# Kernel optimization log

Hardware: AMD Instinct MI355X
Metric: run time of the kernel (lower is better)

## Reference

```python
import jax, jax.numpy as jnp
import numpy as np

N = 100000   # nodes
E = 3200000  # edges
HIGH, LOW, EMB, HID, OUT = 384, 64, 128, 128, 2

def setup_inputs() -> dict:
    key = jax.random.key(0)
    ks = jax.random.split(key, 12)
    def lin(k, fan_in, fan_out):
        bound = 1.0 / np.sqrt(fan_in)
        kw, kb = jax.random.split(k)
        W = jax.random.uniform(kw, (fan_in, fan_out), jnp.float32, -bound, bound)
        b = jax.random.uniform(kb, (fan_out,), jnp.float32, -bound, bound)
        return W, b
    W_emb, b_emb = lin(ks[0], LOW, EMB)
    W1, b1 = lin(ks[1], HIGH + EMB, HID)
    W2, b2 = lin(ks[2], HID, HID)
    W_lin, b_lin = lin(ks[3], HID, OUT)
    return {
        "high_dim_features": jax.random.normal(ks[4], (N, HIGH), jnp.float32),
        "low_dim_features": jax.random.normal(ks[5], (N, LOW), jnp.float32),
        "edge_index": jax.random.randint(ks[6], (2, E), 0, N, jnp.int32),
        "W_emb": W_emb, "b_emb": b_emb,
        "W1": W1, "b1": b1,
        "W2": W2, "b2": b2,
        "W_lin": W_lin, "b_lin": b_lin,
    }

def _gcn_conv(x, W, b, src, dst, dis):
    # GCNConv: add self-loops, symmetric normalization D^-1/2 (A+I) D^-1/2
    xl = x @ W                                   # [N, out]
    norm = dis[src] * dis[dst]                   # [E]
    agg = jax.ops.segment_sum(xl[src] * norm[:, None], dst, num_segments=N)
    agg = agg + xl * (dis * dis)[:, None]        # self-loop term
    return agg + b

def reference(high_dim_features, low_dim_features, edge_index,
              W_emb, b_emb, W1, b1, W2, b2, W_lin, b_lin):
    src, dst = edge_index[0], edge_index[1]
    # degree with self-loops, computed on destination nodes (PyG default)
    deg = jax.ops.segment_sum(jnp.ones((E,), jnp.float32), dst, num_segments=N) + 1.0
    dis = jax.lax.rsqrt(deg)                     # deg >= 1 always

    low_emb = jax.nn.relu(low_dim_features @ W_emb + b_emb)
    x = jnp.concatenate([high_dim_features, low_emb], axis=1)  # [N, HIGH+EMB]
    x = jax.nn.relu(_gcn_conv(x, W1, b1, src, dst, dis))
    # dropout is identity in eval mode
    x = jax.nn.relu(_gcn_conv(x, W2, b2, src, dst, dis))
    x = x @ W_lin + b_lin
    return jax.nn.log_softmax(x, axis=1)
```

## Files before the change

### kernel.cpp

```cpp
#include <hip/hip_runtime.h>

#define HIGH 384
#define LOWD 64
#define EMB  128
#define HID  128

#define BINSHIFT 8
#define SRCBITS  17
#define SRCMASK  0x1FFFF
#define NBLK     256

typedef unsigned int u32;
typedef unsigned short u16;
typedef unsigned char u8;
typedef __attribute__((ext_vector_type(8))) short bf16x8;
typedef __attribute__((ext_vector_type(4))) float f32x4;
typedef __attribute__((ext_vector_type(2))) float f32x2;

__device__ __forceinline__ u32 pack_bf16(float a, float b) {
    u32 ua = __builtin_bit_cast(u32, a);
    u32 ub = __builtin_bit_cast(u32, b);
    ua += 0x7fffu + ((ua >> 16) & 1u);
    ub += 0x7fffu + ((ub >> 16) & 1u);
    return (ua >> 16) | (ub & 0xffff0000u);
}
__device__ __forceinline__ u16 pack1_bf16(float a) {
    u32 ua = __builtin_bit_cast(u32, a);
    ua += 0x7fffu + ((ua >> 16) & 1u);
    return (u16)(ua >> 16);
}
__device__ __forceinline__ u8 pack1_fp8(float a) {
    int r = __builtin_amdgcn_cvt_pk_fp8_f32(a, a, 0, false);
    return (u8)(r & 0xff);
}


__global__ void k_dis(const int* __restrict__ cnt, float* __restrict__ dis, int N) {
    int i = blockIdx.x * 256 + threadIdx.x;
    if (i < N) dis[i] = rsqrtf((float)cnt[i] + 1.0f);
}

__global__ void k_castw_all(const float* __restrict__ W1, u16* __restrict__ Wt1,
                            const float* __restrict__ W2, u16* __restrict__ Wt2,
                            const float* __restrict__ WE, u16* __restrict__ WtE) {
    int i = blockIdx.x * 256 + threadIdx.x;
    if (i < 65536) {
        int k = i >> 7, c = i & 127;
        Wt1[c * 512 + k] = pack1_bf16(W1[i]);
    } else if (i < 81920) {
        int j = i - 65536;
        int k = j >> 7, c = j & 127;
        Wt2[c * 128 + k] = pack1_bf16(W2[j]);
    } else if (i < 90112) {
        int j = i - 81920;
        int k = j >> 7, c = j & 127;
        WtE[c * 64 + k] = pack1_bf16(WE[j]);
    }
}


__global__ __launch_bounds__(256) void k_binhist(const int* __restrict__ dst, int E,
                                                 int* __restrict__ cnts, int NB) {
    __shared__ int hist[512];
    for (int b = threadIdx.x; b < NB; b += 256) hist[b] = 0;
    __syncthreads();
    int CH = (E + gridDim.x - 1) / gridDim.x;
    int e0 = blockIdx.x * CH;
    int e1 = min(E, e0 + CH);
    for (int e = e0 + threadIdx.x; e < e1; e += 256)
        atomicAdd(&hist[dst[e] >> BINSHIFT], 1);
    __syncthreads();
    for (int b = threadIdx.x; b < NB; b += 256)
        cnts[b * NBLK + blockIdx.x] = hist[b];
}

__global__ __launch_bounds__(256) void k_binscatter(const int* __restrict__ src,
                                                    const int* __restrict__ dst, int E,
                                                    const int* __restrict__ cnts,
                                                    u32* __restrict__ packed, int NB) {
    __shared__ int cur[512];
    for (int b = threadIdx.x; b < NB; b += 256) cur[b] = cnts[b * NBLK + blockIdx.x];
    __syncthreads();
    int CH = (E + gridDim.x - 1) / gridDim.x;
    int e0 = blockIdx.x * CH;
    int e1 = min(E, e0 + CH);
    for (int e = e0 + threadIdx.x; e < e1; e += 256) {
        int d = dst[e];
        int s = src[e];
        int bin = d >> BINSHIFT;
        int pos = atomicAdd(&cur[bin], 1);
        packed[pos] = (u32)s | ((u32)(d & 255) << SRCBITS);
    }
}

__global__ __launch_bounds__(256) void k_hist2(const u32* __restrict__ packed,
                                               const int* __restrict__ cnts, int E,
                                               int* __restrict__ cnt, int NB, int N) {
    __shared__ int hist[256];
    int t = threadIdx.x;
    hist[t] = 0;
    __syncthreads();
    int b = blockIdx.x;
    int begin = cnts[b * NBLK];
    int end = (b + 1 < NB) ? cnts[(b + 1) * NBLK] : E;
    for (int e = begin + t; e < end; e += 256)
        atomicAdd(&hist[packed[e] >> SRCBITS], 1);
    __syncthreads();
    int idx = (b << BINSHIFT) + t;
    if (idx < N) cnt[idx] = hist[t];
}

__global__ __launch_bounds__(256) void k_fill2(const u32* __restrict__ packed,
                                               const int* __restrict__ cnts, int E,
                                               const int* __restrict__ row_start,
                                               int* __restrict__ csr, int NB, int N) {
    __shared__ int cur[256];
    int t = threadIdx.x;
    int b = blockIdx.x;
    int base = b << BINSHIFT;
    cur[t] = row_start[min(base + t, N)];
    __syncthreads();
    int begin = cnts[b * NBLK];
    int end = (b + 1 < NB) ? cnts[(b + 1) * NBLK] : E;
    for (int e = begin + t; e < end; e += 256) {
        u32 p = packed[e];
        int pos = atomicAdd(&cur[p >> SRCBITS], 1);
        csr[pos] = (int)((p & SRCMASK) << 5);
    }
}


__global__ void k_scan1(const int* __restrict__ in, int n, int* __restrict__ bsums) {
    __shared__ int sh[256];
    int t = threadIdx.x;
    int base = blockIdx.x * 1024 + t * 4;
    int s = 0;
#pragma unroll
    for (int j = 0; j < 4; j++) { int idx = base + j; s += (idx < n) ? in[idx] : 0; }
    sh[t] = s; __syncthreads();
    for (int off = 128; off > 0; off >>= 1) {
        if (t < off) sh[t] += sh[t + off];
        __syncthreads();
    }
    if (t == 0) bsums[blockIdx.x] = sh[0];
}

__global__ void k_scan2(int* bsums, int nb) {
    if (threadIdx.x == 0 && blockIdx.x == 0) {
        int run = 0;
        for (int i = 0; i < nb; i++) { int v = bsums[i]; bsums[i] = run; run += v; }
    }
}

__global__ void k_scan3_flat(int* __restrict__ data, int n, const int* __restrict__ bsums) {
    __shared__ int sh[256];
    int t = threadIdx.x;
    int base = blockIdx.x * 1024 + t * 4;
    int v[4]; int s = 0;
#pragma unroll
    for (int j = 0; j < 4; j++) { int idx = base + j; v[j] = (idx < n) ? data[idx] : 0; s += v[j]; }
    sh[t] = s; __syncthreads();
    int x = s;
    for (int off = 1; off < 256; off <<= 1) {
        int y = (t >= off) ? sh[t - off] : 0;
        __syncthreads();
        x += y; sh[t] = x;
        __syncthreads();
    }
    int run = bsums[blockIdx.x] + (x - s);
#pragma unroll
    for (int j = 0; j < 4; j++) {
        int idx = base + j;
        if (idx < n) data[idx] = run;
        run += v[j];
    }
}

__global__ void k_scan3_rows(const int* __restrict__ cnt, int N, const int* __restrict__ bsums,
                             int* __restrict__ row_start, int E) {
    __shared__ int sh[256];
    int t = threadIdx.x;
    int base = blockIdx.x * 1024 + t * 4;
    int v[4]; int s = 0;
#pragma unroll
    for (int j = 0; j < 4; j++) { int idx = base + j; v[j] = (idx < N) ? cnt[idx] : 0; s += v[j]; }
    sh[t] = s; __syncthreads();
    int x = s;
    for (int off = 1; off < 256; off <<= 1) {
        int y = (t >= off) ? sh[t - off] : 0;
        __syncthreads();
        x += y; sh[t] = x;
        __syncthreads();
    }
    int run = bsums[blockIdx.x] + (x - s);
#pragma unroll
    for (int j = 0; j < 4; j++) {
        int idx = base + j;
        if (idx < N) row_start[idx] = run;
        run += v[j];
    }
    if (blockIdx.x == 0 && t == 0) row_start[N] = E;
}


template<bool A1BF, bool BIAS, bool RELU, bool SCALE, int OUT>
__global__ __launch_bounds__(256, 6) void k_mgemm(
    const void* __restrict__ A1v, int K1,
    const u32* __restrict__ A2, int K2,
    const u16* __restrict__ Wt,
    const float* __restrict__ bias,
    const float* __restrict__ dis,
    void* __restrict__ Cv, int M)
{
    __shared__ u32 Als[2][64][16];
    __shared__ u32 Bls[2][128][16];

    const int tid = threadIdx.x;
    const int l = tid & 63;
    const int w = tid >> 6;
    const int g = l >> 4;
    const int lr = l & 15;
    const int blockRow = blockIdx.x * 64;
    const int K = K1 + K2;
    const int T = K >> 5;

    const int ar = tid >> 2;
    const int ak = tid & 3;
    int arow = blockRow + ar; if (arow >= M) arow = M - 1;
    const int awb = (ak + ((ar >> 1) & 3)) & 3;

    const int wc = tid >> 1;
    const int wh = tid & 1;
    const int wsw = (wc >> 1) & 3;
    const int wb0 = (wh * 2 + wsw) & 3;
    const int wb1 = (wh * 2 + 1 + wsw) & 3;

    const float* a1f = (const float*)A1v + (size_t)arow * K1;
    const u32*   a1b = (const u32*)A1v + (size_t)arow * (K1 >> 1);
    const u32*   a2b = A2 + (size_t)arow * (K2 >> 1);
    const u32*   wtb = (const u32*)Wt + (size_t)wc * (K >> 1);

    f32x4 acc[8];
#pragma unroll
    for (int j = 0; j < 8; j++) acc[j] = (f32x4)0.f;

    u32 pa[4], wk[8];

    auto load_tile = [&](int k0) {
        if (k0 < K1) {
            if (A1BF) {
                uint4 a = *(const uint4*)(a1b + (k0 >> 1) + ak * 4);
                pa[0] = a.x; pa[1] = a.y; pa[2] = a.z; pa[3] = a.w;
            } else {
                const float* src = a1f + k0 + ak * 8;
                float4 f0 = *(const float4*)(src + 0);
                float4 f1 = *(const float4*)(src + 4);
                pa[0] = pack_bf16(f0.x, f0.y); pa[1] = pack_bf16(f0.z, f0.w);
                pa[2] = pack_bf16(f1.x, f1.y); pa[3] = pack_bf16(f1.z, f1.w);
            }
        } else {
            uint4 a = *(const uint4*)(a2b + ((k0 - K1) >> 1) + ak * 4);
            pa[0] = a.x; pa[1] = a.y; pa[2] = a.z; pa[3] = a.w;
        }
        const u32* srcw = wtb + ((k0 + wh * 16) >> 1);
        uint4 a = *(const uint4*)srcw;
        uint4 b = *(const uint4*)(srcw + 4);
        wk[0] = a.x; wk[1] = a.y; wk[2] = a.z; wk[3] = a.w;
        wk[4] = b.x; wk[5] = b.y; wk[6] = b.z; wk[7] = b.w;
    };
    auto store_tile = [&](int buf) {
        *(uint4*)&Als[buf][ar][awb * 4] = make_uint4(pa[0], pa[1], pa[2], pa[3]);
        *(uint4*)&Bls[buf][wc][wb0 * 4] = make_uint4(wk[0], wk[1], wk[2], wk[3]);
        *(uint4*)&Bls[buf][wc][wb1 * 4] = make_uint4(wk[4], wk[5], wk[6], wk[7]);
    };

    load_tile(0);
    store_tile(0);
    __syncthreads();

    for (int t = 0; t < T; t++) {
        const int cur = t & 1;
        const bool more = (t + 1 < T);
        if (more) load_tile((t + 1) << 5);

        bf16x8 af;
        {
            int r = w * 16 + lr;
            int blk = (g + ((r >> 1) & 3)) & 3;
            af = *(const bf16x8*)&Als[cur][r][blk * 4];
        }
#pragma unroll
        for (int cb = 0; cb < 8; cb++) {
            int c = cb * 16 + lr;
            int blk = (g + ((c >> 1) & 3)) & 3;
            bf16x8 bf = *(const bf16x8*)&Bls[cur][c][blk * 4];
            acc[cb] = __builtin_amdgcn_mfma_f32_16x16x32_bf16(af, bf, acc[cb], 0, 0, 0);
        }
        if (more) store_tile(cur ^ 1);
        __syncthreads();
    }

    float disv[4];
    if (SCALE) {
#pragma unroll
        for (int j = 0; j < 4; j++) {
            int row = blockRow + w * 16 + g * 4 + j;
            disv[j] = (row < M) ? dis[row] : 0.f;
        }
    }
#pragma unroll
    for (int cb = 0; cb < 8; cb++) {
        int col = cb * 16 + lr;
        float bv = BIAS ? bias[col] : 0.f;
#pragma unroll
        for (int j = 0; j < 4; j++) {
            int row = blockRow + w * 16 + g * 4 + j;
            if (row < M) {
                float v = acc[cb][j];
                if (BIAS) v += bv;
                if (SCALE) v *= disv[j];
                if (RELU) v = fmaxf(v, 0.f);
                if (OUT == 0) {
                    ((u16*)Cv)[(size_t)row * 128 + col] = pack1_bf16(v);
                } else {
                    ((u8*)Cv)[(size_t)row * 128 + col] = pack1_fp8(v);
                }
            }
        }
    }
}


template<int MODE>
__global__ __launch_bounds__(256) void k_gatherw(
    const u32* __restrict__ xls32, const int* __restrict__ row_start,
    const int* __restrict__ csr, const float* __restrict__ dis,
    const float* __restrict__ bias, const float* __restrict__ Wl,
    const float* __restrict__ bl, void* __restrict__ outv, int N)
{
    int wave = threadIdx.x >> 6;
    int lane = threadIdx.x & 63;
    int half = lane >> 5;
    int w32 = lane & 31;
    int n = blockIdx.x * 4 + wave;
    if (n >= N) return;
    int jb = row_start[n], je = row_start[n + 1];

    float a0 = 0.f, a1 = 0.f, a2 = 0.f, a3 = 0.f;
    {
        u32 v = xls32[(u32)n * 32 + w32];
        if (half == 0) {
            f32x2 lo = __builtin_amdgcn_cvt_pk_f32_fp8((int)v, false);
            f32x2 hi = __builtin_amdgcn_cvt_pk_f32_fp8((int)v, true);
            a0 = lo.x; a1 = lo.y; a2 = hi.x; a3 = hi.y;
        }
    }

    int j = jb;
    for (; j + 7 < je; j += 8) {
        int c0 = csr[j + 4 * half + 0];
        int c1 = csr[j + 4 * half + 1];
        int c2 = csr[j + 4 * half + 2];
        int c3 = csr[j + 4 * half + 3];
        u32 v0 = xls32[(u32)c0 + w32];
        u32 v1 = xls32[(u32)c1 + w32];
        u32 v2 = xls32[(u32)c2 + w32];
        u32 v3 = xls32[(u32)c3 + w32];
        f32x2 l0 = __builtin_amdgcn_cvt_pk_f32_fp8((int)v0, false);
        f32x2 h0 = __builtin_amdgcn_cvt_pk_f32_fp8((int)v0, true);
        f32x2 l1 = __builtin_amdgcn_cvt_pk_f32_fp8((int)v1, false);
        f32x2 h1 = __builtin_amdgcn_cvt_pk_f32_fp8((int)v1, true);
        f32x2 l2 = __builtin_amdgcn_cvt_pk_f32_fp8((int)v2, false);
        f32x2 h2 = __builtin_amdgcn_cvt_pk_f32_fp8((int)v2, true);
        f32x2 l3 = __builtin_amdgcn_cvt_pk_f32_fp8((int)v3, false);
        f32x2 h3 = __builtin_amdgcn_cvt_pk_f32_fp8((int)v3, true);
        a0 += (l0.x + l1.x) + (l2.x + l3.x);
        a1 += (l0.y + l1.y) + (l2.y + l3.y);
        a2 += (h0.x + h1.x) + (h2.x + h3.x);
        a3 += (h0.y + h1.y) + (h2.y + h3.y);
    }
    for (; j + 3 < je; j += 4) {
        int c0 = csr[j + 2 * half];
        int c1 = csr[j + 2 * half + 1];
        u32 v0 = xls32[(u32)c0 + w32];
        u32 v1 = xls32[(u32)c1 + w32];
        f32x2 l0 = __builtin_amdgcn_cvt_pk_f32_fp8((int)v0, false);
        f32x2 h0 = __builtin_amdgcn_cvt_pk_f32_fp8((int)v0, true);
        f32x2 l1 = __builtin_amdgcn_cvt_pk_f32_fp8((int)v1, false);
        f32x2 h1 = __builtin_amdgcn_cvt_pk_f32_fp8((int)v1, true);
        a0 += l0.x + l1.x; a1 += l0.y + l1.y;
        a2 += h0.x + h1.x; a3 += h0.y + h1.y;
    }
    if (j + 1 < je) {
        int c = csr[j + half];
        u32 v = xls32[(u32)c + w32];
        f32x2 lo = __builtin_amdgcn_cvt_pk_f32_fp8((int)v, false);
        f32x2 hi = __builtin_amdgcn_cvt_pk_f32_fp8((int)v, true);
        a0 += lo.x; a1 += lo.y; a2 += hi.x; a3 += hi.y;
        j += 2;
    }
    if (j < je) {
        int c = csr[j];
        u32 v = xls32[(u32)c + w32];
        if (half == 0) {
            f32x2 lo = __builtin_amdgcn_cvt_pk_f32_fp8((int)v, false);
            f32x2 hi = __builtin_amdgcn_cvt_pk_f32_fp8((int)v, true);
            a0 += lo.x; a1 += lo.y; a2 += hi.x; a3 += hi.y;
        }
    }

    a0 += __shfl(a0, w32 + 32);
    a1 += __shfl(a1, w32 + 32);
    a2 += __shfl(a2, w32 + 32);
    a3 += __shfl(a3, w32 + 32);

    float d = dis[n];
    float4 bv = *(const float4*)&bias[w32 * 4];
    float h0v = fmaxf(fmaf(d, a0, bv.x), 0.f);
    float h1v = fmaxf(fmaf(d, a1, bv.y), 0.f);
    float h2v = fmaxf(fmaf(d, a2, bv.z), 0.f);
    float h3v = fmaxf(fmaf(d, a3, bv.w), 0.f);

    if (MODE == 0) {
        if (half == 0) {
            uint2 pw;
            pw.x = pack_bf16(h0v, h1v);
            pw.y = pack_bf16(h2v, h3v);
            *(uint2*)((u32*)outv + (size_t)n * 64 + w32 * 2) = pw;
        }
    } else {
        float4 q0 = *(const float4*)&Wl[w32 * 8];
        float4 q1 = *(const float4*)&Wl[w32 * 8 + 4];
        float p0 = h0v * q0.x + h1v * q0.z + h2v * q1.x + h3v * q1.z;
        float p1 = h0v * q0.y + h1v * q0.w + h2v * q1.y + h3v * q1.w;
#pragma unroll
        for (int off = 16; off > 0; off >>= 1) {
            p0 += __shfl_down(p0, off);
            p1 += __shfl_down(p1, off);
        }
        if (lane == 0) {
            float z0 = p0 + bl[0], z1 = p1 + bl[1];
            float m = fmaxf(z0, z1);
            float ls = m + logf(expf(z0 - m) + expf(z1 - m));
            float* out = (float*)outv;
            out[(size_t)n * 2 + 0] = z0 - ls;
            out[(size_t)n * 2 + 1] = z1 - ls;
        }
    }
}


extern "C" void kernel_launch(void* const* d_in, const int* in_sizes, int n_in,
                              void* d_out, int out_size, void* d_ws, size_t ws_size,
                              hipStream_t stream) {
    const float* high  = (const float*)d_in[0];
    const float* low   = (const float*)d_in[1];
    const int*   ei    = (const int*)d_in[2];
    const float* W_emb = (const float*)d_in[3];
    const float* b_emb = (const float*)d_in[4];
    const float* W1    = (const float*)d_in[5];
    const float* b1    = (const float*)d_in[6];
    const float* W2    = (const float*)d_in[7];
    const float* b2    = (const float*)d_in[8];
    const float* Wl    = (const float*)d_in[9];
    const float* bl    = (const float*)d_in[10];

    int N = in_sizes[0] / HIGH;
    int E = in_sizes[2] / 2;
    const int* srcp = ei;
    const int* dstp = ei + E;
    float* out = (float*)d_out;

    int NB = (N + 255) >> BINSHIFT;
    int NSCAN = NB * NBLK;

    char* ws = (char*)d_ws;
    size_t off = 0;
    auto alloc = [&](size_t b) { size_t o = off; off += (b + 255) & ~(size_t)255; return o; };
    float* dis       = (float*)(ws + alloc((size_t)N * 4));
    int*   cnt       = (int*)  (ws + alloc((size_t)N * 4));
    int*   row_start = (int*)  (ws + alloc((size_t)(N + 1) * 4));
    int*   bsums     = (int*)  (ws + alloc(4096));
    int*   cnts      = (int*)  (ws + alloc((size_t)NSCAN * 4));
    u32*   packed    = (u32*)  (ws + alloc((size_t)E * 4));
    int*   csr       = (int*)  (ws + alloc((size_t)E * 4));
    u16*   Wt1       = (u16*)  (ws + alloc((size_t)512 * 128 * 2));
    u16*   Wt2       = (u16*)  (ws + alloc((size_t)128 * 128 * 2));
    u16*   WtE       = (u16*)  (ws + alloc((size_t)64 * 128 * 2));
    u16*   bufE      = (u16*)  (ws + alloc((size_t)N * 128 * 2));
    u8*    bufX      = (u8*)   (ws + alloc((size_t)N * 128));
    u16*   bufH      = (u16*)  (ws + alloc((size_t)N * 128 * 2));
    (void)ws_size; (void)n_in; (void)out_size;

    int nbS = (NSCAN + 1023) / 1024;
    int nbN = (N + 1023) / 1024;
    int mt  = (N + 63) / 64;

    k_castw_all<<<(90112 + 255) / 256, 256, 0, stream>>>(W1, Wt1, W2, Wt2, W_emb, WtE);

    k_binhist<<<NBLK, 256, 0, stream>>>(dstp, E, cnts, NB);
    k_scan1<<<nbS, 256, 0, stream>>>(cnts, NSCAN, bsums);
    k_scan2<<<1, 64, 0, stream>>>(bsums, nbS);
    k_scan3_flat<<<nbS, 256, 0, stream>>>(cnts, NSCAN, bsums);
    k_binscatter<<<NBLK, 256, 0, stream>>>(srcp, dstp, E, cnts, packed, NB);
    k_hist2<<<NB, 256, 0, stream>>>(packed, cnts, E, cnt, NB, N);
    k_dis<<<(N + 255) / 256, 256, 0, stream>>>(cnt, dis, N);
    k_scan1<<<nbN, 256, 0, stream>>>(cnt, N, bsums);
    k_scan2<<<1, 64, 0, stream>>>(bsums, nbN);
    k_scan3_rows<<<nbN, 256, 0, stream>>>(cnt, N, bsums, row_start, E);
    k_fill2<<<NB, 256, 0, stream>>>(packed, cnts, E, row_start, csr, NB, N);

    k_mgemm<false, true, true, false, 0><<<mt, 256, 0, stream>>>(
        low, LOWD, (const u32*)bufE, 0, WtE, b_emb, nullptr, bufE, N);
    k_mgemm<false, false, false, true, 1><<<mt, 256, 0, stream>>>(
        high, HIGH, (const u32*)bufE, EMB, Wt1, nullptr, dis, bufX, N);
    k_gatherw<0><<<(N + 3) / 4, 256, 0, stream>>>(
        (const u32*)bufX, row_start, csr, dis, b1, nullptr, nullptr, bufH, N);
    k_mgemm<true, false, false, true, 1><<<mt, 256, 0, stream>>>(
        bufH, HID, (const u32*)bufH, 0, Wt2, nullptr, dis, bufX, N);
    k_gatherw<1><<<(N + 3) / 4, 256, 0, stream>>>(
        (const u32*)bufX, row_start, csr, dis, b2, Wl, bl, out, N);
}
```

Measured before the change: 371.8 us.

## Fuse CSR histogram, scan, dis and fill into one kernel; deepen GEMM prefetch

Replaces the hist2, dis, three-kernel row scan and fill2 sequence with a single per-bin kernel. Each bin's start offset is already known from the bin scan, so a block-local prefix scan yields row_start directly, and the same block writes dis and fills the CSR. This removes five launches and the global cnt round trip. Separately, the mgemm main loop now keeps two register tile buffers so global loads run two tiles ahead. The loop is unrolled by two, which relies on T being even and raises register pressure.

```diff
diff --git a/kernel.cpp b/kernel.cpp
--- a/kernel.cpp
+++ b/kernel.cpp
@@ -34,11 +34,6 @@
     return (u8)(r & 0xff);
 }
 
-
-__global__ void k_dis(const int* __restrict__ cnt, float* __restrict__ dis, int N) {
-    int i = blockIdx.x * 256 + threadIdx.x;
-    if (i < N) dis[i] = rsqrtf((float)cnt[i] + 1.0f);
-}
 
 __global__ void k_castw_all(const float* __restrict__ W1, u16* __restrict__ Wt1,
                             const float* __restrict__ W2, u16* __restrict__ Wt2,
@@ -93,38 +88,48 @@
     }
 }
 
-__global__ __launch_bounds__(256) void k_hist2(const u32* __restrict__ packed,
-                                               const int* __restrict__ cnts, int E,
-                                               int* __restrict__ cnt, int NB, int N) {
+__global__ __launch_bounds__(256) void k_csrbin(
+    const u32* __restrict__ packed, const int* __restrict__ cnts, int E,
+    int* __restrict__ row_start, float* __restrict__ dis,
+    int* __restrict__ csr, int NB, int N)
+{
     __shared__ int hist[256];
+    __shared__ int sc[256];
     int t = threadIdx.x;
-    hist[t] = 0;
-    __syncthreads();
     int b = blockIdx.x;
     int begin = cnts[b * NBLK];
     int end = (b + 1 < NB) ? cnts[(b + 1) * NBLK] : E;
+
+    hist[t] = 0;
+    __syncthreads();
     for (int e = begin + t; e < end; e += 256)
         atomicAdd(&hist[packed[e] >> SRCBITS], 1);
     __syncthreads();
-    int idx = (b << BINSHIFT) + t;
-    if (idx < N) cnt[idx] = hist[t];
-}
-
-__global__ __launch_bounds__(256) void k_fill2(const u32* __restrict__ packed,
-                                               const int* __restrict__ cnts, int E,
-                                               const int* __restrict__ row_start,
-                                               int* __restrict__ csr, int NB, int N) {
-    __shared__ int cur[256];
-    int t = threadIdx.x;
-    int b = blockIdx.x;
-    int base = b << BINSHIFT;
-    cur[t] = row_start[min(base + t, N)];
-    __syncthreads();
-    int begin = cnts[b * NBLK];
-    int end = (b + 1 < NB) ? cnts[(b + 1) * NBLK] : E;
+    int deg = hist[t];
+
+    sc[t] = deg;
+    __syncthreads();
+    int x = deg;
+    for (int off = 1; off < 256; off <<= 1) {
+        int y = (t >= off) ? sc[t - off] : 0;
+        __syncthreads();
+        x += y; sc[t] = x;
+        __syncthreads();
+    }
+    int rs = begin + (x - deg);
+
+    int node = (b << BINSHIFT) + t;
+    if (node < N) {
+        row_start[node] = rs;
+        dis[node] = rsqrtf((float)deg + 1.0f);
+    }
+    if (b == NB - 1 && t == 0) row_start[N] = E;
+
+    hist[t] = rs;
+    __syncthreads();
     for (int e = begin + t; e < end; e += 256) {
         u32 p = packed[e];
-        int pos = atomicAdd(&cur[p >> SRCBITS], 1);
+        int pos = atomicAdd(&hist[p >> SRCBITS], 1);
         csr[pos] = (int)((p & SRCMASK) << 5);
     }
 }
@@ -174,32 +179,6 @@
         if (idx < n) data[idx] = run;
         run += v[j];
     }
-}
-
-__global__ void k_scan3_rows(const int* __restrict__ cnt, int N, const int* __restrict__ bsums,
-                             int* __restrict__ row_start, int E) {
-    __shared__ int sh[256];
-    int t = threadIdx.x;
-    int base = blockIdx.x * 1024 + t * 4;
-    int v[4]; int s = 0;
-#pragma unroll
-    for (int j = 0; j < 4; j++) { int idx = base + j; v[j] = (idx < N) ? cnt[idx] : 0; s += v[j]; }
-    sh[t] = s; __syncthreads();
-    int x = s;
-    for (int off = 1; off < 256; off <<= 1) {
-        int y = (t >= off) ? sh[t - off] : 0;
-        __syncthreads();
-        x += y; sh[t] = x;
-        __syncthreads();
-    }
-    int run = bsums[blockIdx.x] + (x - s);
-#pragma unroll
-    for (int j = 0; j < 4; j++) {
-        int idx = base + j;
-        if (idx < N) row_start[idx] = run;
-        run += v[j];
-    }
-    if (blockIdx.x == 0 && t == 0) row_start[N] = E;
 }
 
 
@@ -244,9 +223,9 @@
 #pragma unroll
     for (int j = 0; j < 8; j++) acc[j] = (f32x4)0.f;
 
-    u32 pa[4], wk[8];
-
-    auto load_tile = [&](int k0) {
+    u32 pa0[4], wk0[8], pa1[4], wk1[8];
+
+    auto load_tile = [&](int k0, u32* pa, u32* wk) {
         if (k0 < K1) {
             if (A1BF) {
                 uint4 a = *(const uint4*)(a1b + (k0 >> 1) + ak * 4);
@@ -268,21 +247,12 @@
         wk[0] = a.x; wk[1] = a.y; wk[2] = a.z; wk[3] = a.w;
         wk[4] = b.x; wk[5] = b.y; wk[6] = b.z; wk[7] = b.w;
     };
-    auto store_tile = [&](int buf) {
+    auto store_tile = [&](int buf, const u32* pa, const u32* wk) {
         *(uint4*)&Als[buf][ar][awb * 4] = make_uint4(pa[0], pa[1], pa[2], pa[3]);
         *(uint4*)&Bls[buf][wc][wb0 * 4] = make_uint4(wk[0], wk[1], wk[2], wk[3]);
         *(uint4*)&Bls[buf][wc][wb1 * 4] = make_uint4(wk[4], wk[5], wk[6], wk[7]);
     };
-
-    load_tile(0);
-    store_tile(0);
-    __syncthreads();
-
-    for (int t = 0; t < T; t++) {
-        const int cur = t & 1;
-        const bool more = (t + 1 < T);
-        if (more) load_tile((t + 1) << 5);
-
+    auto compute = [&](int cur) {
         bf16x8 af;
         {
             int r = w * 16 + lr;
@@ -296,7 +266,21 @@
             bf16x8 bf = *(const bf16x8*)&Bls[cur][c][blk * 4];
             acc[cb] = __builtin_amdgcn_mfma_f32_16x16x32_bf16(af, bf, acc[cb], 0, 0, 0);
         }
-        if (more) store_tile(cur ^ 1);
+    };
+
+    load_tile(0, pa0, wk0);
+    load_tile(32, pa1, wk1);
+    store_tile(0, pa0, wk0);
+    __syncthreads();
+
+    for (int t = 0; t < T; t += 2) {
+        if (t + 2 < T) load_tile((t + 2) << 5, pa0, wk0);
+        compute(0);
+        store_tile(1, pa1, wk1);
+        __syncthreads();
+        if (t + 3 < T) load_tile((t + 3) << 5, pa1, wk1);
+        compute(1);
+        if (t + 2 < T) store_tile(0, pa0, wk0);
         __syncthreads();
     }
 
@@ -478,7 +462,6 @@
     size_t off = 0;
     auto alloc = [&](size_t b) { size_t o = off; off += (b + 255) & ~(size_t)255; return o; };
     float* dis       = (float*)(ws + alloc((size_t)N * 4));
-    int*   cnt       = (int*)  (ws + alloc((size_t)N * 4));
     int*   row_start = (int*)  (ws + alloc((size_t)(N + 1) * 4));
     int*   bsums     = (int*)  (ws + alloc(4096));
     int*   cnts      = (int*)  (ws + alloc((size_t)NSCAN * 4));
@@ -493,7 +476,6 @@
     (void)ws_size; (void)n_in; (void)out_size;
 
     int nbS = (NSCAN + 1023) / 1024;
-    int nbN = (N + 1023) / 1024;
     int mt  = (N + 63) / 64;
 
     k_castw_all<<<(90112 + 255) / 256, 256, 0, stream>>>(W1, Wt1, W2, Wt2, W_emb, WtE);
@@ -503,12 +485,7 @@
     k_scan2<<<1, 64, 0, stream>>>(bsums, nbS);
     k_scan3_flat<<<nbS, 256, 0, stream>>>(cnts, NSCAN, bsums);
     k_binscatter<<<NBLK, 256, 0, stream>>>(srcp, dstp, E, cnts, packed, NB);
-    k_hist2<<<NB, 256, 0, stream>>>(packed, cnts, E, cnt, NB, N);
-    k_dis<<<(N + 255) / 256, 256, 0, stream>>>(cnt, dis, N);
-    k_scan1<<<nbN, 256, 0, stream>>>(cnt, N, bsums);
-    k_scan2<<<1, 64, 0, stream>>>(bsums, nbN);
-    k_scan3_rows<<<nbN, 256, 0, stream>>>(cnt, N, bsums, row_start, E);
-    k_fill2<<<NB, 256, 0, stream>>>(packed, cnts, E, row_start, csr, NB, N);
+    k_csrbin<<<NB, 256, 0, stream>>>(packed, cnts, E, row_start, dis, csr, NB, N);
 
     k_mgemm<false, true, true, false, 0><<<mt, 256, 0, stream>>>(
         low, LOWD, (const u32*)bufE, 0, WtE, b_emb, nullptr, bufE, N);
```

After: 369.9 us. Within noise of the previous version (-0.5%).
